# Optimization experiments

Hardware: AMD Instinct MI355X
Metric: run time of the kernel (lower is better)

## Reference

```python
import jax, jax.numpy as jnp
import numpy as np

N = 50000            # nodes (cells)
E_RAND = 1_600_000   # random edges; self loops appended -> E = E_RAND + N
DIMS = [(512, 384), (384, 256), (256, 128)]  # (in, hidden) per encoder stage
OUT = 128


def setup_inputs() -> dict:
    key = jax.random.key(0)
    ks = jax.random.split(key, 16)
    features = jax.random.normal(ks[0], (N, DIMS[0][0]), dtype=jnp.float32)
    src = jax.random.randint(ks[1], (E_RAND,), 0, N, dtype=jnp.int32)
    dst = jax.random.randint(ks[2], (E_RAND,), 0, N, dtype=jnp.int32)
    loops = jnp.arange(N, dtype=jnp.int32)  # dgl.add_self_loop
    src = jnp.concatenate([src, loops])
    dst = jnp.concatenate([dst, loops])
    inp = {"features": features, "src": src, "dst": dst}
    i = 3
    for s, (din, dout) in enumerate(DIMS):
        inp[f"sage_w{s}"] = jax.random.normal(ks[i], (dout, din), jnp.float32) / np.sqrt(din); i += 1
        inp[f"sage_b{s}"] = jnp.zeros((dout,), jnp.float32)
        inp[f"gc_w{s}"] = jax.random.normal(ks[i], (dout, dout), jnp.float32) / np.sqrt(dout); i += 1
        inp[f"gc_b{s}"] = jnp.zeros((dout,), jnp.float32)
    inp["fc_w"] = jax.random.normal(ks[i], (OUT, DIMS[-1][1]), jnp.float32) / np.sqrt(DIMS[-1][1])
    inp["fc_b"] = jnp.zeros((OUT,), jnp.float32)
    return inp


def reference(features, src, dst,
              sage_w0, sage_b0, gc_w0, gc_b0,
              sage_w1, sage_b1, gc_w1, gc_b1,
              sage_w2, sage_b2, gc_w2, gc_b2,
              fc_w, fc_b):
    ones = jnp.ones((src.shape[0],), jnp.float32)
    in_deg = jax.ops.segment_sum(ones, dst, num_segments=N)
    out_deg = jax.ops.segment_sum(ones, src, num_segments=N)
    # GraphConv norm='both' scalers (clamp degree to >=1, as DGL does)
    inv_src = jnp.where(out_deg > 0, out_deg, 1.0) ** -0.5  # [N]
    inv_dst = jnp.where(in_deg > 0, in_deg, 1.0) ** -0.5    # [N]
    sage_den = (in_deg + 1.0)[:, None]                      # SAGE 'gcn' denominator

    def sage_gcn(h, w, b):
        # DGL SAGEConv aggregator_type='gcn': (sum_neigh + self)/(in_deg+1) -> fc_neigh
        agg = jax.ops.segment_sum(h[src], dst, num_segments=N)
        return ((agg + h) / sage_den) @ w.T + b

    def graph_conv(h, w, b):
        # DGL GraphConv norm='both': D_out^{-1/2} -> sum aggregate -> D_in^{-1/2} -> W
        hn = h * inv_src[:, None]
        agg = jax.ops.segment_sum(hn[src], dst, num_segments=N)
        return (agg * inv_dst[:, None]) @ w.T + b

    params = [(sage_w0, sage_b0, gc_w0, gc_b0),
              (sage_w1, sage_b1, gc_w1, gc_b1),
              (sage_w2, sage_b2, gc_w2, gc_b2)]
    h = features
    for sw, sb, gw, gb in params:
        h = jax.nn.relu(sage_gcn(h, sw, sb))
        h = jax.nn.relu(graph_conv(h, gw, gb))
    return h @ fc_w.T + fc_b
```

## Files before the change

### kernel.cpp

```cpp
#include <hip/hip_runtime.h>
#include <cstddef>
#include <cstdint>


typedef _Float16 h8 __attribute__((ext_vector_type(8)));
typedef _Float16 h4 __attribute__((ext_vector_type(4)));
typedef float f32x4 __attribute__((ext_vector_type(4)));


__global__ __launch_bounds__(256) void deg_kernel(
    const int* __restrict__ src, const int* __restrict__ dst,
    int* __restrict__ in_deg, int* __restrict__ out_deg, int E) {
  int e = blockIdx.x * 256 + threadIdx.x;
  if (e < E) {
    atomicAdd(&in_deg[dst[e]], 1);
    atomicAdd(&out_deg[src[e]], 1);
  }
}

__global__ __launch_bounds__(1024) void scan_kernel(
    const int* __restrict__ deg, int* __restrict__ row_ptr, int n) {
  __shared__ int buf[1024];
  __shared__ int carry_s;
  if (threadIdx.x == 0) carry_s = 0;
  __syncthreads();
  for (int base = 0; base < n; base += 1024) {
    int i = base + (int)threadIdx.x;
    int v = (i < n) ? deg[i] : 0;
    buf[threadIdx.x] = v;
    __syncthreads();
    #pragma unroll
    for (int off = 1; off < 1024; off <<= 1) {
      int t = 0;
      if ((int)threadIdx.x >= off) t = buf[threadIdx.x - off];
      __syncthreads();
      buf[threadIdx.x] += t;
      __syncthreads();
    }
    int incl  = buf[threadIdx.x];
    int carry = carry_s;
    int total = buf[1023];
    __syncthreads();
    if (i < n) row_ptr[i] = carry + incl - v;
    if (threadIdx.x == 0) carry_s = carry + total;
    __syncthreads();
  }
  if (threadIdx.x == 0) row_ptr[n] = carry_s;
}

__global__ __launch_bounds__(256) void scatter_kernel(
    const int* __restrict__ src, const int* __restrict__ dst,
    const int* __restrict__ row_ptr, int* __restrict__ cnt,
    int* __restrict__ csr, int E) {
  int e = blockIdx.x * 256 + threadIdx.x;
  if (e < E) {
    int d = dst[e];
    int pos = row_ptr[d] + atomicAdd(&cnt[d], 1);
    csr[pos] = src[e];
  }
}

__global__ __launch_bounds__(256) void scaler_kernel(
    const int* __restrict__ in_deg, const int* __restrict__ out_deg,
    float* __restrict__ inv_src, float* __restrict__ inv_dst,
    float* __restrict__ inv_den, int n) {
  int i = blockIdx.x * 256 + threadIdx.x;
  if (i < n) {
    float od = (float)out_deg[i];
    float id = (float)in_deg[i];
    inv_src[i] = rsqrtf(od > 0.f ? od : 1.0f);
    inv_dst[i] = rsqrtf(id > 0.f ? id : 1.0f);
    inv_den[i] = 1.0f / (id + 1.0f);
  }
}


__global__ __launch_bounds__(256) void cvt_kernel(
    const float* __restrict__ in, _Float16* __restrict__ out,
    long n_in, long n_pad) {
  long i = ((long)blockIdx.x * 256 + (long)threadIdx.x) * 4;
  if (i >= n_pad) return;
  float4 v = (i < n_in) ? *(const float4*)(in + i) : make_float4(0.f, 0.f, 0.f, 0.f);
  h4 h = {(_Float16)v.x, (_Float16)v.y, (_Float16)v.z, (_Float16)v.w};
  *(h4*)(out + i) = h;
}


template <typename OutT>
__global__ __launch_bounds__(256) void hgemm(
    const _Float16* __restrict__ A, const _Float16* __restrict__ W,
    OutT* __restrict__ C, int Mstore, int K, int Nc,
    const float* __restrict__ row_scale, const float* __restrict__ bias) {
  __shared__ _Float16 As[128 * 32];
  __shared__ _Float16 Bs[128 * 32];
  const int tid = threadIdx.x;
  const int bm = blockIdx.x * 128, bn = blockIdx.y * 128;
  const int wave = tid >> 6, lane = tid & 63;
  const int wm = (wave & 1) * 64, wn = (wave >> 1) * 64;
  const int lrow = lane & 15, lq = lane >> 4;

  const int r0 = tid >> 2;
  const int cc = (tid & 3) * 8;
  const _Float16* Ag = A + (size_t)(bm + r0) * K + cc;
  const _Float16* Wg = W + (size_t)(bn + r0) * K + cc;
  const size_t rs64 = (size_t)64 * K;

  f32x4 acc[4][4];
  #pragma unroll
  for (int i = 0; i < 4; ++i)
    #pragma unroll
    for (int j = 0; j < 4; ++j) acc[i][j] = (f32x4){0.f, 0.f, 0.f, 0.f};

  for (int k0 = 0; k0 < K; k0 += 32) {
    uint4 a0 = *(const uint4*)(Ag + k0);
    uint4 a1 = *(const uint4*)(Ag + rs64 + k0);
    uint4 b0 = *(const uint4*)(Wg + k0);
    uint4 b1 = *(const uint4*)(Wg + rs64 + k0);
    __syncthreads();
    *(uint4*)(As + r0 * 32 + cc) = a0;
    *(uint4*)(As + (64 + r0) * 32 + cc) = a1;
    *(uint4*)(Bs + r0 * 32 + cc) = b0;
    *(uint4*)(Bs + (64 + r0) * 32 + cc) = b1;
    __syncthreads();
    h8 af[4], bf[4];
    #pragma unroll
    for (int i = 0; i < 4; ++i)
      af[i] = *(const h8*)(As + (wm + i * 16 + lrow) * 32 + lq * 8);
    #pragma unroll
    for (int j = 0; j < 4; ++j)
      bf[j] = *(const h8*)(Bs + (wn + j * 16 + lrow) * 32 + lq * 8);
    #pragma unroll
    for (int i = 0; i < 4; ++i)
      #pragma unroll
      for (int j = 0; j < 4; ++j)
        acc[i][j] = __builtin_amdgcn_mfma_f32_16x16x32_f16(af[i], bf[j], acc[i][j], 0, 0, 0);
  }

  #pragma unroll
  for (int i = 0; i < 4; ++i) {
    #pragma unroll
    for (int r = 0; r < 4; ++r) {
      const int m = bm + wm + i * 16 + lq * 4 + r;
      if (m < Mstore) {
        const float rsc = row_scale ? row_scale[m] : 1.0f;
        OutT* crow = C + (size_t)m * Nc + bn + wn + lrow;
        #pragma unroll
        for (int j = 0; j < 4; ++j) {
          float v = acc[i][j][r] * rsc;
          if (bias) v += bias[bn + wn + j * 16 + lrow];
          crow[j * 16] = (OutT)v;
        }
      }
    }
  }
}


template <int D, bool SELF>
__global__ __launch_bounds__(256) void agg_h(
    const _Float16* __restrict__ Z, const int* __restrict__ row_ptr,
    const int* __restrict__ csr, const float* __restrict__ out_scale,
    const float* __restrict__ bias, _Float16* __restrict__ out, int n) {
  constexpr int CH = D / 8;
  constexpr int GROUP = 16;
  constexpr int NV = CH / GROUP;
  const int gid = threadIdx.x >> 4;
  const int lane = threadIdx.x & 15;
  const int node = blockIdx.x * 16 + gid;
  if (node >= n) return;

  const int rs = row_ptr[node], re = row_ptr[node + 1];

  float acc[NV][8];
  #pragma unroll
  for (int v = 0; v < NV; ++v)
    #pragma unroll
    for (int q = 0; q < 8; ++q) acc[v][q] = 0.f;

  for (int e = rs; e < re; e += GROUP) {
    int m = re - e; if (m > GROUP) m = GROUP;
    int eid = (lane < m) ? csr[e + lane] : 0;
    for (int j = 0; j < m; ++j) {
      int s = __shfl(eid, j, GROUP);
      const h8* zr = (const h8*)(Z + (size_t)s * D);
      #pragma unroll
      for (int v = 0; v < NV; ++v) {
        h8 t = zr[lane + v * GROUP];
        #pragma unroll
        for (int q = 0; q < 8; ++q) acc[v][q] += (float)t[q];
      }
    }
  }

  const float osc = out_scale[node];
  const h8* zs = (const h8*)(Z + (size_t)node * D);
  _Float16* orow = out + (size_t)node * D;
  #pragma unroll
  for (int v = 0; v < NV; ++v) {
    const int idx = lane + v * GROUP;
    if (SELF) {
      h8 t = zs[idx];
      #pragma unroll
      for (int q = 0; q < 8; ++q) acc[v][q] += (float)t[q];
    }
    h8 r;
    #pragma unroll
    for (int q = 0; q < 8; ++q) {
      float x = acc[v][q] * osc + bias[idx * 8 + q];
      r[q] = (_Float16)fmaxf(x, 0.f);
    }
    *(h8*)(orow + idx * 8) = r;
  }
}


static void launch_cvt(const float* in, _Float16* out, long n_in, long n_pad,
                       hipStream_t st) {
  long thr = n_pad / 4;
  cvt_kernel<<<(int)((thr + 255) / 256), 256, 0, st>>>(in, out, n_in, n_pad);
}

extern "C" void kernel_launch(void* const* d_in, const int* in_sizes, int n_in,
                              void* d_out, int out_size, void* d_ws, size_t ws_size,
                              hipStream_t stream) {
  const float* features = (const float*)d_in[0];
  const int*   src      = (const int*)d_in[1];
  const int*   dst      = (const int*)d_in[2];
  const float* wsrc[7] = {(const float*)d_in[3],  (const float*)d_in[5],
                          (const float*)d_in[7],  (const float*)d_in[9],
                          (const float*)d_in[11], (const float*)d_in[13],
                          (const float*)d_in[15]};
  const float* sb[3] = {(const float*)d_in[4],  (const float*)d_in[8],  (const float*)d_in[12]};
  const float* gb[3] = {(const float*)d_in[6],  (const float*)d_in[10], (const float*)d_in[14]};
  const float* fc_b  = (const float*)d_in[16];

  const int N = in_sizes[0] / 512;
  const int E = in_sizes[1];
  const int MB = (N + 127) / 128;
  const int Mpad = MB * 128;

  const int wcnt[7] = {384 * 512, 384 * 384, 256 * 384, 256 * 256,
                       128 * 256, 128 * 128, 128 * 128};

  char* ws = (char*)d_ws;
  _Float16* featH = (_Float16*)ws;
  _Float16* hA    = featH + (size_t)Mpad * 512;
  _Float16* hB    = hA + (size_t)Mpad * 384;
  _Float16* wH[7];
  {
    _Float16* p = hB + (size_t)Mpad * 384;
    for (int i = 0; i < 7; ++i) { wH[i] = p; p += wcnt[i]; }
  }
  int* csr     = (int*)(wH[6] + wcnt[6]);
  int* rp      = csr + E;
  int* in_dg   = rp + (N + 1);
  int* out_dg  = in_dg + N;
  int* cnt     = out_dg + N;
  float* inv_src = (float*)(cnt + N);
  float* inv_dst = inv_src + N;
  float* inv_den = inv_dst + N;

  size_t totw = 0; for (int i = 0; i < 7; ++i) totw += wcnt[i];
  size_t needed = ((size_t)Mpad * (512 + 384 + 384) + totw) * 2 +
                  ((size_t)E + (N + 1) + 6 * (size_t)N) * 4;
  if (ws_size < needed) return;

  (void)hipMemsetAsync(in_dg, 0, sizeof(int) * 3 * (size_t)N, stream);

  const int eb = (E + 255) / 256;
  const int nb = (N + 255) / 256;
  deg_kernel<<<eb, 256, 0, stream>>>(src, dst, in_dg, out_dg, E);
  scan_kernel<<<1, 1024, 0, stream>>>(in_dg, rp, N);
  scatter_kernel<<<eb, 256, 0, stream>>>(src, dst, rp, cnt, csr, E);
  scaler_kernel<<<nb, 256, 0, stream>>>(in_dg, out_dg, inv_src, inv_dst, inv_den, N);

  launch_cvt(features, featH, (long)N * 512, (long)Mpad * 512, stream);
  for (int i = 0; i < 7; ++i) launch_cvt(wsrc[i], wH[i], wcnt[i], wcnt[i], stream);

  const int dout[3] = {384, 256, 128};
  const _Float16* h = featH;
  int K = 512;
  for (int s = 0; s < 3; ++s) {
    const int D = dout[s];
    dim3 gg(MB, D / 128);
    const int ab = (N + 15) / 16;
    hgemm<_Float16><<<gg, 256, 0, stream>>>(h, wH[2 * s], hB, Mpad, K, D, nullptr, nullptr);
    if (D == 384)      agg_h<384, true><<<ab, 256, 0, stream>>>(hB, rp, csr, inv_den, sb[s], hA, N);
    else if (D == 256) agg_h<256, true><<<ab, 256, 0, stream>>>(hB, rp, csr, inv_den, sb[s], hA, N);
    else               agg_h<128, true><<<ab, 256, 0, stream>>>(hB, rp, csr, inv_den, sb[s], hA, N);
    hgemm<_Float16><<<gg, 256, 0, stream>>>(hA, wH[2 * s + 1], hB, Mpad, D, D, inv_src, nullptr);
    if (D == 384)      agg_h<384, false><<<ab, 256, 0, stream>>>(hB, rp, csr, inv_dst, gb[s], hA, N);
    else if (D == 256) agg_h<256, false><<<ab, 256, 0, stream>>>(hB, rp, csr, inv_dst, gb[s], hA, N);
    else               agg_h<128, false><<<ab, 256, 0, stream>>>(hB, rp, csr, inv_dst, gb[s], hA, N);
    h = hA;
    K = D;
  }
  dim3 gf(MB, 1);
  hgemm<float><<<gf, 256, 0, stream>>>(h, wH[6], (float*)d_out, N, 128, 128, nullptr, fc_b);
}
```

Measured before the change: 1.363 ms.

## Pad CSR rows to multiples of four, unroll gather, use direct global-to-LDS loads

Each node's CSR row is padded to a multiple of four entries, and the pad slots point to a zeroed dummy row at index Mpad. This lets the aggregation kernel issue four neighbor-row loads at once with no tail handling, raising memory-level parallelism in the gather. The GEMM now stages A and W tiles with global_load_lds instead of going through registers. The cost is extra padding edges, an additional fill kernel and memsets for the dummy rows.

```diff
diff --git a/kernel.cpp b/kernel.cpp
--- a/kernel.cpp
+++ b/kernel.cpp
@@ -6,6 +6,11 @@
 typedef _Float16 h8 __attribute__((ext_vector_type(8)));
 typedef _Float16 h4 __attribute__((ext_vector_type(4)));
 typedef float f32x4 __attribute__((ext_vector_type(4)));
+
+#define GLD_LDS16(gptr, lptr)                                                  \
+  __builtin_amdgcn_global_load_lds(                                            \
+      (const __attribute__((address_space(1))) void*)(gptr),                   \
+      (__attribute__((address_space(3))) void*)(lptr), 16, 0, 0)
 
 
 __global__ __launch_bounds__(256) void deg_kernel(
@@ -26,7 +31,7 @@
   __syncthreads();
   for (int base = 0; base < n; base += 1024) {
     int i = base + (int)threadIdx.x;
-    int v = (i < n) ? deg[i] : 0;
+    int v = (i < n) ? ((deg[i] + 3) & ~3) : 0;
     buf[threadIdx.x] = v;
     __syncthreads();
     #pragma unroll
@@ -57,6 +62,16 @@
     int d = dst[e];
     int pos = row_ptr[d] + atomicAdd(&cnt[d], 1);
     csr[pos] = src[e];
+  }
+}
+
+__global__ __launch_bounds__(256) void pad_fill_kernel(
+    const int* __restrict__ row_ptr, const int* __restrict__ deg,
+    int* __restrict__ csr, int n, int dummy) {
+  int i = blockIdx.x * 256 + threadIdx.x;
+  if (i < n) {
+    int s = row_ptr[i] + deg[i], e = row_ptr[i + 1];
+    for (int p = s; p < e; ++p) csr[p] = dummy;
   }
 }
 
@@ -99,11 +114,16 @@
   const int wm = (wave & 1) * 64, wn = (wave >> 1) * 64;
   const int lrow = lane & 15, lq = lane >> 4;
 
-  const int r0 = tid >> 2;
-  const int cc = (tid & 3) * 8;
-  const _Float16* Ag = A + (size_t)(bm + r0) * K + cc;
-  const _Float16* Wg = W + (size_t)(bn + r0) * K + cc;
-  const size_t rs64 = (size_t)64 * K;
+  const int colh = (lane & 3) * 8;
+  const int arow = wave * 16 + (lane >> 2);
+  const _Float16* Ag  = A + (size_t)(bm + arow) * K + colh;
+  const _Float16* Ag2 = A + (size_t)(bm + 64 + arow) * K + colh;
+  const _Float16* Wg  = W + (size_t)(bn + arow) * K + colh;
+  const _Float16* Wg2 = W + (size_t)(bn + 64 + arow) * K + colh;
+  _Float16* lA  = As + wave * 512;
+  _Float16* lA2 = As + 64 * 32 + wave * 512;
+  _Float16* lB  = Bs + wave * 512;
+  _Float16* lB2 = Bs + 64 * 32 + wave * 512;
 
   f32x4 acc[4][4];
   #pragma unroll
@@ -112,15 +132,11 @@
     for (int j = 0; j < 4; ++j) acc[i][j] = (f32x4){0.f, 0.f, 0.f, 0.f};
 
   for (int k0 = 0; k0 < K; k0 += 32) {
-    uint4 a0 = *(const uint4*)(Ag + k0);
-    uint4 a1 = *(const uint4*)(Ag + rs64 + k0);
-    uint4 b0 = *(const uint4*)(Wg + k0);
-    uint4 b1 = *(const uint4*)(Wg + rs64 + k0);
-    __syncthreads();
-    *(uint4*)(As + r0 * 32 + cc) = a0;
-    *(uint4*)(As + (64 + r0) * 32 + cc) = a1;
-    *(uint4*)(Bs + r0 * 32 + cc) = b0;
-    *(uint4*)(Bs + (64 + r0) * 32 + cc) = b1;
+    __syncthreads();
+    GLD_LDS16(Ag + k0, lA);
+    GLD_LDS16(Ag2 + k0, lA2);
+    GLD_LDS16(Wg + k0, lB);
+    GLD_LDS16(Wg2 + k0, lB2);
     __syncthreads();
     h8 af[4], bf[4];
     #pragma unroll
@@ -161,9 +177,8 @@
     const _Float16* __restrict__ Z, const int* __restrict__ row_ptr,
     const int* __restrict__ csr, const float* __restrict__ out_scale,
     const float* __restrict__ bias, _Float16* __restrict__ out, int n) {
-  constexpr int CH = D / 8;
   constexpr int GROUP = 16;
-  constexpr int NV = CH / GROUP;
+  constexpr int NV = D / 8 / GROUP;
   const int gid = threadIdx.x >> 4;
   const int lane = threadIdx.x & 15;
   const int node = blockIdx.x * 16 + gid;
@@ -179,16 +194,28 @@
 
   for (int e = rs; e < re; e += GROUP) {
     int m = re - e; if (m > GROUP) m = GROUP;
-    int eid = (lane < m) ? csr[e + lane] : 0;
-    for (int j = 0; j < m; ++j) {
-      int s = __shfl(eid, j, GROUP);
-      const h8* zr = (const h8*)(Z + (size_t)s * D);
+    int eid = (e + lane < re) ? csr[e + lane] : 0;
+    for (int j = 0; j < m; j += 4) {
+      const int s0 = __shfl(eid, j + 0, GROUP);
+      const int s1 = __shfl(eid, j + 1, GROUP);
+      const int s2 = __shfl(eid, j + 2, GROUP);
+      const int s3 = __shfl(eid, j + 3, GROUP);
+      const h8* z0 = (const h8*)(Z + (size_t)s0 * D);
+      const h8* z1 = (const h8*)(Z + (size_t)s1 * D);
+      const h8* z2 = (const h8*)(Z + (size_t)s2 * D);
+      const h8* z3 = (const h8*)(Z + (size_t)s3 * D);
+      h8 t0[NV], t1[NV], t2[NV], t3[NV];
       #pragma unroll
       for (int v = 0; v < NV; ++v) {
-        h8 t = zr[lane + v * GROUP];
+        const int idx = lane + v * GROUP;
+        t0[v] = z0[idx]; t1[v] = z1[idx]; t2[v] = z2[idx]; t3[v] = z3[idx];
+      }
+      #pragma unroll
+      for (int v = 0; v < NV; ++v)
         #pragma unroll
-        for (int q = 0; q < 8; ++q) acc[v][q] += (float)t[q];
-      }
+        for (int q = 0; q < 8; ++q)
+          acc[v][q] += ((float)t0[v][q] + (float)t1[v][q]) +
+                       ((float)t2[v][q] + (float)t3[v][q]);
     }
   }
 
@@ -238,6 +265,7 @@
   const int E = in_sizes[1];
   const int MB = (N + 127) / 128;
   const int Mpad = MB * 128;
+  const int Epad_max = E + 3 * N + 64;
 
   const int wcnt[7] = {384 * 512, 384 * 384, 256 * 384, 256 * 256,
                        128 * 256, 128 * 128, 128 * 128};
@@ -248,11 +276,11 @@
   _Float16* hB    = hA + (size_t)Mpad * 384;
   _Float16* wH[7];
   {
-    _Float16* p = hB + (size_t)Mpad * 384;
+    _Float16* p = hB + (size_t)(Mpad + 1) * 384;
     for (int i = 0; i < 7; ++i) { wH[i] = p; p += wcnt[i]; }
   }
   int* csr     = (int*)(wH[6] + wcnt[6]);
-  int* rp      = csr + E;
+  int* rp      = csr + Epad_max;
   int* in_dg   = rp + (N + 1);
   int* out_dg  = in_dg + N;
   int* cnt     = out_dg + N;
@@ -261,17 +289,19 @@
   float* inv_den = inv_dst + N;
 
   size_t totw = 0; for (int i = 0; i < 7; ++i) totw += wcnt[i];
-  size_t needed = ((size_t)Mpad * (512 + 384 + 384) + totw) * 2 +
-                  ((size_t)E + (N + 1) + 6 * (size_t)N) * 4;
+  size_t needed = ((size_t)Mpad * (512 + 384) + (size_t)(Mpad + 1) * 384 + totw) * 2 +
+                  ((size_t)Epad_max + (N + 1) + 6 * (size_t)N) * 4;
   if (ws_size < needed) return;
 
   (void)hipMemsetAsync(in_dg, 0, sizeof(int) * 3 * (size_t)N, stream);
+  (void)hipMemsetAsync(hA + (size_t)N * 384, 0, (size_t)(Mpad - N) * 384 * 2, stream);
 
   const int eb = (E + 255) / 256;
   const int nb = (N + 255) / 256;
   deg_kernel<<<eb, 256, 0, stream>>>(src, dst, in_dg, out_dg, E);
   scan_kernel<<<1, 1024, 0, stream>>>(in_dg, rp, N);
   scatter_kernel<<<eb, 256, 0, stream>>>(src, dst, rp, cnt, csr, E);
+  pad_fill_kernel<<<nb, 256, 0, stream>>>(rp, in_dg, csr, N, Mpad);
   scaler_kernel<<<nb, 256, 0, stream>>>(in_dg, out_dg, inv_src, inv_dst, inv_den, N);
 
   launch_cvt(features, featH, (long)N * 512, (long)Mpad * 512, stream);
@@ -284,6 +314,7 @@
     const int D = dout[s];
     dim3 gg(MB, D / 128);
     const int ab = (N + 15) / 16;
+    (void)hipMemsetAsync(hB + (size_t)Mpad * D, 0, (size_t)D * 2, stream);
     hgemm<_Float16><<<gg, 256, 0, stream>>>(h, wH[2 * s], hB, Mpad, K, D, nullptr, nullptr);
     if (D == 384)      agg_h<384, true><<<ab, 256, 0, stream>>>(hB, rp, csr, inv_den, sb[s], hA, N);
     else if (D == 256) agg_h<256, true><<<ab, 256, 0, stream>>>(hB, rp, csr, inv_den, sb[s], hA, N);
```

Result: no change. 1.368 ms (+0.4%).
